# Kernel optimization log

Hardware: AMD Instinct MI355X
Metric: run time of the kernel (lower is better)

The kernel has to match this reference:

```python
import jax, jax.numpy as jnp
import numpy as np

LR = 0.01            # learning_rate
PC = 0.001           # pred_clipping
WC = 5.0             # weight_clipping
_LO = float(np.log(PC / (1.0 - PC)))   # logit(pred_clipping)
_HI = -_LO                              # logit(1 - pred_clipping)


def setup_inputs() -> dict:
    B, S, I, CTX, M, C = 64, 1023, 1024, 784, 4, 1  # S = size-1 (bias row), C = num_classes->1
    key = jax.random.key(0)
    k = jax.random.split(key, 6)
    logit = jax.random.normal(k[0], (B, I, C), jnp.float32)
    context = jax.random.normal(k[1], (B, CTX), jnp.float32)
    target = jax.random.uniform(k[2], (B, C), dtype=jnp.float32)
    cm = jax.random.normal(k[3], (C, S, M, CTX), jnp.float32)
    cm = cm / jnp.linalg.norm(cm, axis=-1, keepdims=True)          # unit-norm context maps
    cb = jax.random.normal(k[4], (C, S, M, 1), jnp.float32)        # context bias
    weights = jnp.full((C, S, 2 ** M, I), 1.0 / I, jnp.float32)    # per-context weight table
    bias = jax.random.uniform(k[5], (1, 1, C), jnp.float32, _LO, _HI)
    return {"logit": logit, "context": context, "target": target,
            "context_maps": cm, "context_bias": cb, "weights": weights, "bias": bias}


def reference(logit, context, target, context_maps, context_bias, weights, bias):
    C, S, M, _ = context_maps.shape
    B = context.shape[0]
    # halfspace hashing of the context -> per-(class, neuron, sample) weight-table index
    dist = jnp.einsum('csmk,bk->csmb', context_maps, context)      # [C,S,M,B]
    bits = (dist > context_bias).astype(jnp.int32)
    conv = (2 ** jnp.arange(M, dtype=jnp.int32))[:, None]          # [M,1]
    idx = jnp.sum(bits * conv, axis=-2)                            # [C,S,B] in [0, 2^M)
    ci = jnp.arange(C)[:, None, None]
    si = jnp.arange(S)[None, :, None]
    sel = weights[ci, si, idx]                                     # gather -> [C,S,B,I]
    # batched dot product (torch code does full matmul + diagonal; this is the same math)
    out = jnp.clip(jnp.einsum('csbi,bic->csb', sel, logit), _LO, _HI)
    out_bsc = out.transpose(2, 1, 0)                               # [B,S,C]
    # online weight update (target branch): gather-compute-scatter
    diff = jax.nn.sigmoid(out_bsc) - target[:, None, :]            # [B,S,C]
    upd = LR * diff[..., None] * logit.transpose(0, 2, 1)[:, None, :, :]  # [B,S,C,I]
    new_sel = jnp.clip(sel - upd.transpose(2, 1, 0, 3), -WC, WC)   # [C,S,B,I]
    new_weights = weights.at[ci, si, idx].set(new_sel)             # scatter
    # prepend constant bias neuron
    out_logits = jnp.concatenate([jnp.broadcast_to(bias, (B, 1, C)), out_bsc], axis=1)  # [B,S+1,C]
    return out_logits, new_weights
```

## Files before the change

kernel.cpp:

```cpp
#include <hip/hip_runtime.h>
#include <math.h>

typedef unsigned long long u64;
typedef __attribute__((ext_vector_type(8))) short bf16x8;
typedef __attribute__((ext_vector_type(4))) float f32x4;

#define S_DIM 1023
#define B_DIM 64
#define I_DIM 1024
#define CTX_DIM 784
#define CTX4 196
#define NWROWS 16
#define NTASK (S_DIM * NWROWS)

#define LR_C 0.01f
#define WC_C 5.0f
#define LO_C (-6.906754778648554f)
#define HI_C ( 6.906754778648554f)

__device__ __forceinline__ float dot4(float4 a, float4 b) {
    return a.x * b.x + a.y * b.y + a.z * b.z + a.w * b.w;
}

__device__ __forceinline__ float4 upd4(float4 w, float4 a, float c) {
    float4 r;
    r.x = fminf(fmaxf(w.x - c * a.x, -WC_C), WC_C);
    r.y = fminf(fmaxf(w.y - c * a.y, -WC_C), WC_C);
    r.z = fminf(fmaxf(w.z - c * a.z, -WC_C), WC_C);
    r.w = fminf(fmaxf(w.w - c * a.w, -WC_C), WC_C);
    return r;
}

__device__ __forceinline__ short f2bf(float f) {
    union { float f; unsigned u; } cv; cv.f = f;
    unsigned r = cv.u + 0x7fffu + ((cv.u >> 16) & 1u);
    return (short)(r >> 16);
}

__global__ __launch_bounds__(256) void prep_pack_kernel(
    const float* __restrict__ context,
    const float* __restrict__ bias,
    const float* __restrict__ logit,
    float4* __restrict__ ctxT4,
    short* __restrict__ pack_b,
    float* __restrict__ out_logits)
{
    const int blk = blockIdx.x;
    const int t = threadIdx.x;
    if (blk < 49) {
        int g = blk * 256 + t;
        int k4 = g >> 6;
        int b  = g & 63;
        ctxT4[g] = *(const float4*)(context + (size_t)b * CTX_DIM + k4 * 4);
        if (g < B_DIM) out_logits[(size_t)g * (S_DIM + 1)] = bias[0];
    } else {
        int g = (blk - 49) * 256 + t;
        int l  = g & 63;
        int kb = (g >> 6) & 31;
        int nt = g >> 11;
        int b  = nt * 16 + (l & 15);
        int i0 = kb * 32 + (l >> 4) * 8;
        const float* src = logit + (size_t)b * I_DIM + i0;
        bf16x8 v;
        #pragma unroll
        for (int j = 0; j < 8; ++j) v[j] = f2bf(src[j]);
        *(bf16x8*)(pack_b + (size_t)g * 8) = v;
    }
}

__global__ __launch_bounds__(256, 4) void gln_dots_kernel(
    const float* __restrict__ logit,
    const float* __restrict__ target,
    const float* __restrict__ weights,
    const float* __restrict__ cm,
    const float* __restrict__ cb,
    const float4* __restrict__ ctxT4,
    const short* __restrict__ pack_b,
    float* __restrict__ out_logits,
    int*   __restrict__ lastb_g,
    float* __restrict__ coef_g)
{
    __shared__ short Abf[NWROWS * I_DIM];
    __shared__ float red[4][4][64];
    __shared__ int   bits[4][64];
    __shared__ float cb_lds[4];
    __shared__ u64   mask_lds[NWROWS];
    __shared__ int   lastb_lds[NWROWS];

    const int s  = blockIdx.x;
    const int t  = threadIdx.x;
    const int wv = t >> 6;
    const int l  = t & 63;

    if (t < 4) cb_lds[t] = cb[s * 4 + t];

    const float4* W4 = (const float4*)(weights + (size_t)s * (NWROWS * I_DIM));
    #pragma unroll
    for (int j = 0; j < NWROWS; ++j) {
        float4 w = W4[t + j * 256];
        int slot = j * 128 + ((t >> 1) ^ (j & 7));
        short4 v;
        v.x = f2bf(w.x); v.y = f2bf(w.y); v.z = f2bf(w.z); v.w = f2bf(w.w);
        *(short4*)(Abf + slot * 8 + (t & 1) * 4) = v;
    }

    {
        const int b = t & 63;
        const int q = __builtin_amdgcn_readfirstlane(t >> 6);
        const float4* cmr = (const float4*)(cm + (size_t)s * 4 * CTX_DIM);
        float a0 = 0.f, a1 = 0.f, a2 = 0.f, a3 = 0.f;
        const int k0 = q * 49;
        #pragma unroll 7
        for (int kk = 0; kk < 49; ++kk) {
            int k4 = k0 + kk;
            float4 c4 = ctxT4[k4 * 64 + b];
            a0 += dot4(cmr[k4], c4);
            a1 += dot4(cmr[CTX4 + k4], c4);
            a2 += dot4(cmr[2 * CTX4 + k4], c4);
            a3 += dot4(cmr[3 * CTX4 + k4], c4);
        }
        red[q][0][b] = a0;
        red[q][1][b] = a1;
        red[q][2][b] = a2;
        red[q][3][b] = a3;
    }
    __syncthreads();
    {
        int m = t >> 6, bb = t & 63;
        float sum = red[0][m][bb] + red[1][m][bb] + red[2][m][bb] + red[3][m][bb];
        bits[m][bb] = (sum > cb_lds[m]) ? 1 : 0;
    }
    __syncthreads();
    if (t < B_DIM) {
        int v = bits[0][t] + 2 * bits[1][t] + 4 * bits[2][t] + 8 * bits[3][t];
        u64 my = 0;
        #pragma unroll
        for (int kk = 0; kk < NWROWS; ++kk) {
            u64 mk = __ballot(v == kk);
            if (t == kk) my = mk;
        }
        if (t < NWROWS) {
            int lb = my ? (63 - __clzll(my)) : -1;
            mask_lds[t]  = my;
            lastb_lds[t] = lb;
            lastb_g[s * NWROWS + t] = lb;
        }
    }
    __syncthreads();

    const int row = l & 15;
    const int q2  = l >> 4;
    const int sw  = row & 7;
    const int base_slot = row * 128;
    const bf16x8* Bb = (const bf16x8*)pack_b + (size_t)wv * 2048 + l;
    f32x4 acc = {0.f, 0.f, 0.f, 0.f};
    #pragma unroll 8
    for (int kb = 0; kb < 32; ++kb) {
        bf16x8 af = *(const bf16x8*)(Abf + 8 * (base_slot + ((kb * 4 + q2) ^ sw)));
        bf16x8 bfr = Bb[(size_t)kb * 64];
        acc = __builtin_amdgcn_mfma_f32_16x16x32_bf16(af, bfr, acc, 0, 0, 0);
    }

    const int col = wv * 16 + (l & 15);
    #pragma unroll
    for (int j = 0; j < 4; ++j) {
        int r = q2 * 4 + j;
        u64 m = mask_lds[r];
        if ((m >> col) & 1) {
            float o = fminf(fmaxf(acc[j], LO_C), HI_C);
            out_logits[(size_t)col * (S_DIM + 1) + s + 1] = o;
            if (col == lastb_lds[r])
                coef_g[s * NWROWS + r] = LR_C * (1.0f / (1.0f + expf(-o)) - target[col]);
        }
    }
}

__global__ __launch_bounds__(256) void gln_upd_kernel(
    const float* __restrict__ logit,
    const float* __restrict__ weights,
    const int*   __restrict__ lastb_g,
    const float* __restrict__ coef_g,
    float* __restrict__ new_weights)
{
    const int total = NTASK * 256;
    const int stride = gridDim.x * 256;
    for (int g = blockIdx.x * 256 + threadIdx.x; g < total; g += stride) {
        const int task = g >> 8;
        const int off  = g & 255;
        const int lb   = lastb_g[task];
        float4 w = ((const float4*)weights)[g];
        float4 r;
        if (lb < 0) {
            r = w;
        } else {
            const float c = coef_g[task];
            float4 a = ((const float4*)logit)[lb * 256 + off];
            r = upd4(w, a, c);
        }
        ((float4*)new_weights)[g] = r;
    }
}

extern "C" void kernel_launch(void* const* d_in, const int* in_sizes, int n_in,
                              void* d_out, int out_size, void* d_ws, size_t ws_size,
                              hipStream_t stream) {
    const float* logit   = (const float*)d_in[0];
    const float* context = (const float*)d_in[1];
    const float* target  = (const float*)d_in[2];
    const float* cm      = (const float*)d_in[3];
    const float* cb      = (const float*)d_in[4];
    const float* weights = (const float*)d_in[5];
    const float* bias    = (const float*)d_in[6];

    float* out_logits  = (float*)d_out;
    float* new_weights = out_logits + (size_t)B_DIM * (S_DIM + 1);

    char* ws = (char*)d_ws;
    float4* ctxT4   = (float4*)ws;   ws += (size_t)CTX4 * B_DIM * 16;
    short*  packb   = (short*)ws;    ws += (size_t)4 * 32 * 64 * 8 * 2;
    int*    lastb_g = (int*)ws;      ws += (size_t)NTASK * 4;
    float*  coef_g  = (float*)ws;

    prep_pack_kernel<<<81, 256, 0, stream>>>(context, bias, logit, ctxT4, packb, out_logits);
    gln_dots_kernel<<<S_DIM, 256, 0, stream>>>(logit, target, weights, cm, cb,
                                               ctxT4, packb, out_logits,
                                               lastb_g, coef_g);
    gln_upd_kernel<<<8192, 256, 0, stream>>>(logit, weights, lastb_g, coef_g, new_weights);
}
```

Before: 64.28 us.

## Split hashing into its own kernel and stream weights directly into MFMA

Moves the context halfspace hashing (and logit packing) into a separate kernel that writes per-row masks and last-batch indices to global memory. The dot kernel then no longer stages the weight rows into LDS. Each lane loads fp32 weights straight from global, converts them to bf16 in registers and feeds the MFMA. This removes the LDS staging and block barriers from the dot kernel and frees LDS for occupancy, at the cost of an extra kernel launch and global round trips for the mask data.

```diff
diff --git a/kernel.cpp b/kernel.cpp
--- a/kernel.cpp
+++ b/kernel.cpp
@@ -37,24 +37,37 @@
     return (short)(r >> 16);
 }
 
-__global__ __launch_bounds__(256) void prep_pack_kernel(
+__global__ __launch_bounds__(256) void prep_kernel(
     const float* __restrict__ context,
     const float* __restrict__ bias,
+    float4* __restrict__ ctxT4,
+    float* __restrict__ out_logits)
+{
+    int g = blockIdx.x * 256 + threadIdx.x;
+    int k4 = g >> 6;
+    int b  = g & 63;
+    ctxT4[g] = *(const float4*)(context + (size_t)b * CTX_DIM + k4 * 4);
+    if (g < B_DIM) out_logits[(size_t)g * (S_DIM + 1)] = bias[0];
+}
+
+__global__ __launch_bounds__(256) void mega_kernel(
     const float* __restrict__ logit,
-    float4* __restrict__ ctxT4,
+    const float* __restrict__ cm,
+    const float* __restrict__ cb,
+    const float4* __restrict__ ctxT4,
     short* __restrict__ pack_b,
-    float* __restrict__ out_logits)
-{
+    u64* __restrict__ mask_g,
+    int* __restrict__ lastb_g)
+{
+    __shared__ float red[4][4][64];
+    __shared__ int   bits[4][64];
+    __shared__ float cb_lds[4];
+
     const int blk = blockIdx.x;
     const int t = threadIdx.x;
-    if (blk < 49) {
+
+    if (blk < 32) {
         int g = blk * 256 + t;
-        int k4 = g >> 6;
-        int b  = g & 63;
-        ctxT4[g] = *(const float4*)(context + (size_t)b * CTX_DIM + k4 * 4);
-        if (g < B_DIM) out_logits[(size_t)g * (S_DIM + 1)] = bias[0];
-    } else {
-        int g = (blk - 49) * 256 + t;
         int l  = g & 63;
         int kb = (g >> 6) & 31;
         int nt = g >> 11;
@@ -65,72 +78,40 @@
         #pragma unroll
         for (int j = 0; j < 8; ++j) v[j] = f2bf(src[j]);
         *(bf16x8*)(pack_b + (size_t)g * 8) = v;
-    }
-}
-
-__global__ __launch_bounds__(256, 4) void gln_dots_kernel(
-    const float* __restrict__ logit,
-    const float* __restrict__ target,
-    const float* __restrict__ weights,
-    const float* __restrict__ cm,
-    const float* __restrict__ cb,
-    const float4* __restrict__ ctxT4,
-    const short* __restrict__ pack_b,
-    float* __restrict__ out_logits,
-    int*   __restrict__ lastb_g,
-    float* __restrict__ coef_g)
-{
-    __shared__ short Abf[NWROWS * I_DIM];
-    __shared__ float red[4][4][64];
-    __shared__ int   bits[4][64];
-    __shared__ float cb_lds[4];
-    __shared__ u64   mask_lds[NWROWS];
-    __shared__ int   lastb_lds[NWROWS];
-
-    const int s  = blockIdx.x;
-    const int t  = threadIdx.x;
-    const int wv = t >> 6;
-    const int l  = t & 63;
-
+        return;
+    }
+
+    const int s = blk - 32;
     if (t < 4) cb_lds[t] = cb[s * 4 + t];
 
-    const float4* W4 = (const float4*)(weights + (size_t)s * (NWROWS * I_DIM));
-    #pragma unroll
-    for (int j = 0; j < NWROWS; ++j) {
-        float4 w = W4[t + j * 256];
-        int slot = j * 128 + ((t >> 1) ^ (j & 7));
-        short4 v;
-        v.x = f2bf(w.x); v.y = f2bf(w.y); v.z = f2bf(w.z); v.w = f2bf(w.w);
-        *(short4*)(Abf + slot * 8 + (t & 1) * 4) = v;
-    }
-
-    {
-        const int b = t & 63;
-        const int q = __builtin_amdgcn_readfirstlane(t >> 6);
-        const float4* cmr = (const float4*)(cm + (size_t)s * 4 * CTX_DIM);
-        float a0 = 0.f, a1 = 0.f, a2 = 0.f, a3 = 0.f;
-        const int k0 = q * 49;
-        #pragma unroll 7
-        for (int kk = 0; kk < 49; ++kk) {
-            int k4 = k0 + kk;
-            float4 c4 = ctxT4[k4 * 64 + b];
-            a0 += dot4(cmr[k4], c4);
-            a1 += dot4(cmr[CTX4 + k4], c4);
-            a2 += dot4(cmr[2 * CTX4 + k4], c4);
-            a3 += dot4(cmr[3 * CTX4 + k4], c4);
-        }
-        red[q][0][b] = a0;
-        red[q][1][b] = a1;
-        red[q][2][b] = a2;
-        red[q][3][b] = a3;
-    }
+    const int b = t & 63;
+    const int q = __builtin_amdgcn_readfirstlane(t >> 6);
+    const float4* cmr = (const float4*)(cm + (size_t)s * 4 * CTX_DIM);
+
+    float a0 = 0.f, a1 = 0.f, a2 = 0.f, a3 = 0.f;
+    const int k0 = q * 49;
+    #pragma unroll 7
+    for (int kk = 0; kk < 49; ++kk) {
+        int k4 = k0 + kk;
+        float4 c4 = ctxT4[k4 * 64 + b];
+        a0 += dot4(cmr[k4], c4);
+        a1 += dot4(cmr[CTX4 + k4], c4);
+        a2 += dot4(cmr[2 * CTX4 + k4], c4);
+        a3 += dot4(cmr[3 * CTX4 + k4], c4);
+    }
+    red[q][0][b] = a0;
+    red[q][1][b] = a1;
+    red[q][2][b] = a2;
+    red[q][3][b] = a3;
     __syncthreads();
+
     {
         int m = t >> 6, bb = t & 63;
         float sum = red[0][m][bb] + red[1][m][bb] + red[2][m][bb] + red[3][m][bb];
         bits[m][bb] = (sum > cb_lds[m]) ? 1 : 0;
     }
     __syncthreads();
+
     if (t < B_DIM) {
         int v = bits[0][t] + 2 * bits[1][t] + 4 * bits[2][t] + 8 * bits[3][t];
         u64 my = 0;
@@ -140,36 +121,53 @@
             if (t == kk) my = mk;
         }
         if (t < NWROWS) {
-            int lb = my ? (63 - __clzll(my)) : -1;
-            mask_lds[t]  = my;
-            lastb_lds[t] = lb;
-            lastb_g[s * NWROWS + t] = lb;
-        }
-    }
-    __syncthreads();
-
-    const int row = l & 15;
-    const int q2  = l >> 4;
-    const int sw  = row & 7;
-    const int base_slot = row * 128;
+            mask_g[s * NWROWS + t]  = my;
+            lastb_g[s * NWROWS + t] = my ? (63 - __clzll(my)) : -1;
+        }
+    }
+}
+
+__global__ __launch_bounds__(256, 4) void gln_dots_kernel(
+    const float* __restrict__ logit,
+    const float* __restrict__ target,
+    const float* __restrict__ weights,
+    const u64*   __restrict__ mask_g,
+    const int*   __restrict__ lastb_g,
+    const short* __restrict__ pack_b,
+    float* __restrict__ out_logits,
+    float* __restrict__ coef_g)
+{
+    const int s  = blockIdx.x;
+    const int t  = threadIdx.x;
+    const int wv = t >> 6;
+    const int l  = t & 63;
+
+    const float* Abase = weights + (size_t)s * (NWROWS * I_DIM)
+                       + (size_t)(l & 15) * I_DIM + ((l >> 4) * 8);
     const bf16x8* Bb = (const bf16x8*)pack_b + (size_t)wv * 2048 + l;
+
     f32x4 acc = {0.f, 0.f, 0.f, 0.f};
-    #pragma unroll 8
+    #pragma unroll 4
     for (int kb = 0; kb < 32; ++kb) {
-        bf16x8 af = *(const bf16x8*)(Abf + 8 * (base_slot + ((kb * 4 + q2) ^ sw)));
+        float4 x = *(const float4*)(Abase + kb * 32);
+        float4 y = *(const float4*)(Abase + kb * 32 + 4);
+        bf16x8 af;
+        af[0] = f2bf(x.x); af[1] = f2bf(x.y); af[2] = f2bf(x.z); af[3] = f2bf(x.w);
+        af[4] = f2bf(y.x); af[5] = f2bf(y.y); af[6] = f2bf(y.z); af[7] = f2bf(y.w);
         bf16x8 bfr = Bb[(size_t)kb * 64];
         acc = __builtin_amdgcn_mfma_f32_16x16x32_bf16(af, bfr, acc, 0, 0, 0);
     }
 
     const int col = wv * 16 + (l & 15);
+    const int q2  = l >> 4;
     #pragma unroll
     for (int j = 0; j < 4; ++j) {
         int r = q2 * 4 + j;
-        u64 m = mask_lds[r];
+        u64 m = mask_g[s * NWROWS + r];
         if ((m >> col) & 1) {
             float o = fminf(fmaxf(acc[j], LO_C), HI_C);
             out_logits[(size_t)col * (S_DIM + 1) + s + 1] = o;
-            if (col == lastb_lds[r])
+            if (col == lastb_g[s * NWROWS + r])
                 coef_g[s * NWROWS + r] = LR_C * (1.0f / (1.0f + expf(-o)) - target[col]);
         }
     }
@@ -218,12 +216,14 @@
     char* ws = (char*)d_ws;
     float4* ctxT4   = (float4*)ws;   ws += (size_t)CTX4 * B_DIM * 16;
     short*  packb   = (short*)ws;    ws += (size_t)4 * 32 * 64 * 8 * 2;
+    u64*    mask_g  = (u64*)ws;      ws += (size_t)NTASK * 8;
     int*    lastb_g = (int*)ws;      ws += (size_t)NTASK * 4;
     float*  coef_g  = (float*)ws;
 
-    prep_pack_kernel<<<81, 256, 0, stream>>>(context, bias, logit, ctxT4, packb, out_logits);
-    gln_dots_kernel<<<S_DIM, 256, 0, stream>>>(logit, target, weights, cm, cb,
-                                               ctxT4, packb, out_logits,
-                                               lastb_g, coef_g);
+    prep_kernel<<<CTX4 * B_DIM / 256, 256, 0, stream>>>(context, bias, ctxT4, out_logits);
+    mega_kernel<<<32 + S_DIM, 256, 0, stream>>>(logit, cm, cb, ctxT4,
+                                                packb, mask_g, lastb_g);
+    gln_dots_kernel<<<S_DIM, 256, 0, stream>>>(logit, target, weights, mask_g, lastb_g,
+                                               packb, out_logits, coef_g);
     gln_upd_kernel<<<8192, 256, 0, stream>>>(logit, weights, lastb_g, coef_g, new_weights);
 }
```

Result: slower. 83.14 us (+29.3%).
